# Performance work log

Hardware: AMD Instinct MI355X
Metric: run time of the kernel (lower is better)

Reference implementation:

```python
import jax, jax.numpy as jnp
import numpy as np

B, S, H, NH, HD = 2, 2048, 2048, 32, 64
ROPE_THETA = 10000.0


def _rope_tables(seq_len, head_dim, theta):
    inv_freq = 1.0 / (theta ** (jnp.arange(0, head_dim, 2, dtype=jnp.float32) / head_dim))
    t = jnp.arange(seq_len, dtype=jnp.float32)
    freqs = jnp.outer(t, inv_freq)                 # [S, HD/2]
    emb = jnp.concatenate([freqs, freqs], axis=-1)  # [S, HD]
    return jnp.cos(emb), jnp.sin(emb)


def setup_inputs() -> dict:
    key = jax.random.key(0)
    ks = jax.random.split(key, 6)
    cos, sin = _rope_tables(S, HD, ROPE_THETA)
    scale = 0.02
    return {
        "hidden_states": jax.random.normal(ks[0], (B, S, H), dtype=jnp.float32),
        "attention_mask": jnp.zeros((B, S), dtype=jnp.float32),
        "cos": cos,
        "sin": sin,
        "Wq": jax.random.normal(ks[1], (H, H), dtype=jnp.float32) * scale,
        "Wk": jax.random.normal(ks[2], (H, H), dtype=jnp.float32) * scale,
        "Wv": jax.random.normal(ks[3], (H, H), dtype=jnp.float32) * scale,
        "Wo": jax.random.normal(ks[4], (H, H), dtype=jnp.float32) * scale,
    }


def _rotate_half(x):
    x1, x2 = jnp.split(x, 2, axis=-1)
    return jnp.concatenate([-x2, x1], axis=-1)


def reference(hidden_states, attention_mask, cos, sin, Wq, Wk, Wv, Wo):
    b, s, _ = hidden_states.shape
    # QKV projections (nn.Linear: x @ W.T), reshape to [B, NH, S, HD]
    def proj(W):
        y = hidden_states @ W.T
        return y.reshape(b, s, NH, HD).transpose(0, 2, 1, 3)
    q, k, v = proj(Wq), proj(Wk), proj(Wv)
    # RoPE (HF rotate_half convention); cos/sin: [S, HD] -> broadcast [1,1,S,HD]
    c = cos[None, None, :, :]
    sn = sin[None, None, :, :]
    q = q * c + _rotate_half(q) * sn
    k = k * c + _rotate_half(k) * sn
    # attention: [B, NH, S, S]
    scores = jnp.einsum("bhqd,bhkd->bhqk", q, k) / jnp.sqrt(jnp.float32(HD))
    scores = scores + attention_mask[:, None, None, :]
    probs = jax.nn.softmax(scores, axis=-1)
    out = jnp.einsum("bhqk,bhkd->bhqd", probs, v)
    out = out.transpose(0, 2, 1, 3).reshape(b, s, NH * HD)
    return out @ Wo.T
```

## Files before the change

kernel.cpp:

```cpp
#include <hip/hip_runtime.h>
#include <stdint.h>
#include <math.h>

#define NB 2
#define SS 2048
#define HH 2048
#define NHH 32
#define HDD 64
#define MM (NB*SS)

typedef __attribute__((ext_vector_type(8))) short short8;
typedef __attribute__((ext_vector_type(4))) short short4v;
typedef __attribute__((ext_vector_type(4))) float f32x4;

#define GLOBAL_AS const __attribute__((address_space(1))) void*
#define LDS_AS __attribute__((address_space(3))) void*

static __device__ __forceinline__ short rne_bf16(float x) {
    uint32_t u = __builtin_bit_cast(uint32_t, x);
    u += 0x7FFFu + ((u >> 16) & 1u);
    return (short)(u >> 16);
}
static __device__ __forceinline__ float bf16f(short h) {
    return __builtin_bit_cast(float, (uint32_t)((uint16_t)h) << 16);
}
static __device__ __forceinline__ uint32_t cvt_pk_bf16(float a, float b) {
    uint32_t r;
    asm("v_cvt_pk_bf16_f32 %0, %1, %2" : "=v"(r) : "v"(a), "v"(b));
    return r;
}
static __device__ __forceinline__ float fast_exp2(float x) {
    float r;
    asm("v_exp_f32 %0, %1" : "=v"(r) : "v"(x));
    return r;
}

#define N4X  2097152
#define N4W  1048576
__global__ void __launch_bounds__(256)
k_cvt_all(const float* __restrict__ X, const float* __restrict__ Wq,
          const float* __restrict__ Wk, const float* __restrict__ Wv,
          const float* __restrict__ Wo,
          short* __restrict__ Xh, short* __restrict__ Wqh, short* __restrict__ Wkh,
          short* __restrict__ Wvh, short* __restrict__ Woh, short* __restrict__ Wol)
{
    int i = blockIdx.x * blockDim.x + threadIdx.x;
    const float* src;
    short* dst;
    int j = i;
    if (i < N4X)                { src = X;  dst = Xh;  }
    else if (i < N4X + N4W)     { src = Wq; dst = Wqh; j = i - N4X; }
    else if (i < N4X + 2*N4W)   { src = Wk; dst = Wkh; j = i - N4X - N4W; }
    else if (i < N4X + 3*N4W)   { src = Wv; dst = Wvh; j = i - N4X - 2*N4W; }
    else {
        j = i - N4X - 3*N4W;
        float4 f = reinterpret_cast<const float4*>(Wo)[j];
        short4v h, l;
        h.x = rne_bf16(f.x); l.x = rne_bf16(f.x - bf16f(h.x));
        h.y = rne_bf16(f.y); l.y = rne_bf16(f.y - bf16f(h.y));
        h.z = rne_bf16(f.z); l.z = rne_bf16(f.z - bf16f(h.z));
        h.w = rne_bf16(f.w); l.w = rne_bf16(f.w - bf16f(h.w));
        reinterpret_cast<short4v*>(Woh)[j] = h;
        reinterpret_cast<short4v*>(Wol)[j] = l;
        return;
    }
    float4 f = reinterpret_cast<const float4*>(src)[j];
    short4v o;
    o.x = rne_bf16(f.x); o.y = rne_bf16(f.y);
    o.z = rne_bf16(f.z); o.w = rne_bf16(f.w);
    reinterpret_cast<short4v*>(dst)[j] = o;
}

__global__ void __launch_bounds__(256, 2)
k_gemm_qkv(const short* __restrict__ X,
           const short* __restrict__ Wqh, const short* __restrict__ Wkh, const short* __restrict__ Wvh,
           const float* __restrict__ cosT, const float* __restrict__ sinT,
           short* __restrict__ Qr, short* __restrict__ Kr, short* __restrict__ Vt)
{
    __shared__ short lA[128 * 64];
    __shared__ short lBq[128 * 64];
    __shared__ short lBk[128 * 64];
    __shared__ short lBv[128 * 64];
    const int tid = threadIdx.x;
    const int lane = tid & 63;
    const int wave = tid >> 6;
    const int lrow = lane & 15;
    const int quad = lane >> 4;
    const int swz = lrow & 7;

    const int lin = blockIdx.y * 16 + blockIdx.x;
    const int pos = lin >> 3;
    const int nblk = ((lin & 7) * 2 + (pos & 1)) * 128;
    const int mblk = (pos >> 1) * 128;
    const int m0 = mblk + (wave >> 1) * 64;
    const int n0 = nblk + (wave & 1) * 64;
    const int mw = (wave >> 1) * 64;
    const int nw = (wave & 1) * 64;

    const int srow = wave * 32 + (lane >> 3);
    const int skc = ((lane & 7) ^ (lane >> 3)) * 8;
    const short* gA = X   + (size_t)(mblk + srow) * HH + skc;
    const short* gQ = Wqh + (size_t)(nblk + srow) * HH + skc;
    const short* gK = Wkh + (size_t)(nblk + srow) * HH + skc;
    const short* gV = Wvh + (size_t)(nblk + srow) * HH + skc;
    const int lofs = wave * 2048;

    f32x4 acc[3][4][4];
    #pragma unroll
    for (int z = 0; z < 3; z++)
        #pragma unroll
        for (int i = 0; i < 4; i++)
            #pragma unroll
            for (int j = 0; j < 4; j++) acc[z][i][j] = 0.f;

    #pragma unroll 1
    for (int k0 = 0; k0 < HH; k0 += 64) {
        __syncthreads();
        #pragma unroll
        for (int j = 0; j < 4; j++) {
            size_t go = (size_t)j * 8 * HH + k0;
            int lo = lofs + j * 512;
            __builtin_amdgcn_global_load_lds((GLOBAL_AS)(gA + go), (LDS_AS)(&lA[lo]),  16, 0, 0);
            __builtin_amdgcn_global_load_lds((GLOBAL_AS)(gQ + go), (LDS_AS)(&lBq[lo]), 16, 0, 0);
            __builtin_amdgcn_global_load_lds((GLOBAL_AS)(gK + go), (LDS_AS)(&lBk[lo]), 16, 0, 0);
            __builtin_amdgcn_global_load_lds((GLOBAL_AS)(gV + go), (LDS_AS)(&lBv[lo]), 16, 0, 0);
        }
        __syncthreads();

        const short* lBz[3] = { lBq, lBk, lBv };
        #pragma unroll
        for (int kk = 0; kk < 2; kk++) {
            const int csl = ((kk * 4 + quad) ^ swz) * 8;
            short8 a[4];
            #pragma unroll
            for (int mt = 0; mt < 4; mt++)
                a[mt] = *reinterpret_cast<const short8*>(&lA[(mw + mt * 16 + lrow) * 64 + csl]);
            #pragma unroll
            for (int z = 0; z < 3; z++) {
                short8 b[4];
                #pragma unroll
                for (int nt = 0; nt < 4; nt++)
                    b[nt] = *reinterpret_cast<const short8*>(&lBz[z][(nw + nt * 16 + lrow) * 64 + csl]);
                #pragma unroll
                for (int mt = 0; mt < 4; mt++)
                    #pragma unroll
                    for (int nt = 0; nt < 4; nt++)
                        acc[z][mt][nt] = __builtin_amdgcn_mfma_f32_16x16x32_bf16(a[mt], b[nt], acc[z][mt][nt], 0, 0, 0);
            }
        }
    }

    const float QSCL = 0.18033688011112042f;

    #pragma unroll
    for (int z = 0; z < 3; z++) {
        #pragma unroll
        for (int mt = 0; mt < 4; mt++) {
            #pragma unroll
            for (int r = 0; r < 4; r++) {
                int row = m0 + mt * 16 + quad * 4 + r;
                int b_i = row >> 11;
                int s_i = row & (SS - 1);
                #pragma unroll
                for (int nt = 0; nt < 4; nt++) {
                    int col = n0 + nt * 16 + lrow;
                    int h_i = col >> 6;
                    int d_i = col & 63;
                    float v = acc[z][mt][nt][r];
                    if (z < 2) {
                        float pair = (nt & 2) ? acc[z][mt][nt - 2][r] : -acc[z][mt][nt + 2][r];
                        float c = cosT[s_i * HDD + d_i];
                        float sn = sinT[s_i * HDD + d_i];
                        v = v * c + pair * sn;
                        if (z == 0) v *= QSCL;
                        short* dst = (z == 0) ? Qr : Kr;
                        dst[(((size_t)b_i * NHH + h_i) * SS + s_i) * HDD + d_i] = rne_bf16(v);
                    } else {
                        Vt[(((size_t)b_i * NHH + h_i) * HDD + d_i) * SS + s_i] = rne_bf16(v);
                    }
                }
            }
        }
    }
}

__global__ void __launch_bounds__(256, 2)
k_attn(const short* __restrict__ Qr, const short* __restrict__ Kr, const short* __restrict__ Vt,
       const float* __restrict__ mask,
       short* __restrict__ Ah, short* __restrict__ Al)
{
    __shared__ short plds[4][4096];
    __shared__ short ldsK[2][4096];
    __shared__ short ldsV[2][4096];
    const int lane = threadIdx.x & 63;
    const int wave = threadIdx.x >> 6;
    const int lrow = lane & 15;
    const int quad = lane >> 4;
    const int aofs = lrow & 7;
    const int b = blockIdx.x >> 5;
    const int h = blockIdx.x & 31;
    const int q0w = blockIdx.y * 256 + wave * 64;

    const size_t bh = (size_t)b * NHH + h;
    const short* Qbase = Qr + bh * SS * HDD;
    const short* Kbase = Kr + bh * SS * HDD;
    const short* Vbase = Vt + bh * (size_t)HDD * SS;
    const float* mrow = mask + b * SS;
    char* cb = (char*)&plds[wave][0];

    const int strow = lane >> 3;
    const int stch  = (lane & 7) ^ strow;
    const short* Kst0 = Kbase + (size_t)(wave * 16 + strow)     * HDD + stch * 8;
    const short* Kst1 = Kbase + (size_t)(wave * 16 + 8 + strow) * HDD + stch * 8;
    const short* Vst0 = Vbase + (size_t)(wave * 16 + strow)     * SS  + stch * 8;
    const short* Vst1 = Vbase + (size_t)(wave * 16 + 8 + strow) * SS  + stch * 8;
    const int ldst0 = wave * 1024;
    const int ldst1 = wave * 1024 + 512;

#define STAGE_KV(buf, kk) do { \
    __builtin_amdgcn_global_load_lds((GLOBAL_AS)(Kst0 + (size_t)(kk) * HDD), (LDS_AS)(&ldsK[buf][ldst0]), 16, 0, 0); \
    __builtin_amdgcn_global_load_lds((GLOBAL_AS)(Kst1 + (size_t)(kk) * HDD), (LDS_AS)(&ldsK[buf][ldst1]), 16, 0, 0); \
    __builtin_amdgcn_global_load_lds((GLOBAL_AS)(Vst0 + (kk)), (LDS_AS)(&ldsV[buf][ldst0]), 16, 0, 0); \
    __builtin_amdgcn_global_load_lds((GLOBAL_AS)(Vst1 + (kk)), (LDS_AS)(&ldsV[buf][ldst1]), 16, 0, 0); \
} while (0)

    short8 qf[4][2];
    #pragma unroll
    for (int nt = 0; nt < 4; nt++)
        #pragma unroll
        for (int c = 0; c < 2; c++)
            qf[nt][c] = *reinterpret_cast<const short8*>(
                Qbase + (size_t)(q0w + nt * 16 + lrow) * HDD + c * 32 + quad * 8);

    short8 onesf;
    #pragma unroll
    for (int i = 0; i < 8; i++) onesf[i] = (short)0x3F80;

    f32x4 oacc[4][4];
    f32x4 lacc[4];
    #pragma unroll
    for (int i = 0; i < 4; i++) {
        lacc[i] = 0.f;
        #pragma unroll
        for (int j = 0; j < 4; j++) oacc[i][j] = 0.f;
    }

    const float L2E = 1.44269504f;

    STAGE_KV(0, 0);
    asm volatile("s_waitcnt vmcnt(0)" ::: "memory");
    __syncthreads();

    int cur = 0;
    #pragma unroll 1
    for (int k0 = 0; k0 < SS; k0 += 64) {
        if (k0 + 64 < SS) STAGE_KV(cur ^ 1, k0 + 64);

        short8 kf[4][2];
        #pragma unroll
        for (int kt = 0; kt < 4; kt++)
            #pragma unroll
            for (int c = 0; c < 2; c++)
                kf[kt][c] = *reinterpret_cast<const short8*>(
                    &ldsK[cur][(kt * 16 + lrow) * 64 + (((4 * c + quad) ^ aofs) * 8)]);

        f32x4 sacc[4][4];
        #pragma unroll
        for (int kt = 0; kt < 4; kt++)
            #pragma unroll
            for (int nt = 0; nt < 4; nt++) {
                f32x4 z4 = 0.f;
                z4 = __builtin_amdgcn_mfma_f32_16x16x32_bf16(kf[kt][0], qf[nt][0], z4, 0, 0, 0);
                sacc[kt][nt] = __builtin_amdgcn_mfma_f32_16x16x32_bf16(kf[kt][1], qf[nt][1], z4, 0, 0, 0);
            }

        asm volatile("s_waitcnt lgkmcnt(0)" ::: "memory");

        #pragma unroll
        for (int kt = 0; kt < 4; kt++) {
            float4 mk = *reinterpret_cast<const float4*>(mrow + k0 + kt * 16 + quad * 4);
            float m0v = mk.x * L2E, m1v = mk.y * L2E, m2v = mk.z * L2E, m3v = mk.w * L2E;
            #pragma unroll
            for (int nt = 0; nt < 4; nt++) {
                float p0 = fast_exp2(sacc[kt][nt][0] + m0v);
                float p1 = fast_exp2(sacc[kt][nt][1] + m1v);
                float p2 = fast_exp2(sacc[kt][nt][2] + m2v);
                float p3 = fast_exp2(sacc[kt][nt][3] + m3v);
                uint2 w;
                w.x = cvt_pk_bf16(p0, p1);
                w.y = cvt_pk_bf16(p2, p3);
                *reinterpret_cast<uint2*>(
                    cb + (nt * 16 + lrow) * 128 +
                    (((2 * kt + (quad >> 1)) ^ aofs) * 16) + (quad & 1) * 8) = w;
            }
        }

        asm volatile("s_waitcnt lgkmcnt(0)" ::: "memory");

        #pragma unroll
        for (int c = 0; c < 2; c++) {
            short8 pf[4], vf[4];
            #pragma unroll
            for (int mt = 0; mt < 4; mt++)
                pf[mt] = *reinterpret_cast<const short8*>(
                    cb + (mt * 16 + lrow) * 128 + (((4 * c + quad) ^ aofs) * 16));
            #pragma unroll
            for (int dt = 0; dt < 4; dt++)
                vf[dt] = *reinterpret_cast<const short8*>(
                    &ldsV[cur][(dt * 16 + lrow) * 64 + (((4 * c + quad) ^ aofs) * 8)]);
            #pragma unroll
            for (int mt = 0; mt < 4; mt++) {
                lacc[mt] = __builtin_amdgcn_mfma_f32_16x16x32_bf16(pf[mt], onesf, lacc[mt], 0, 0, 0);
                #pragma unroll
                for (int dt = 0; dt < 4; dt++)
                    oacc[mt][dt] = __builtin_amdgcn_mfma_f32_16x16x32_bf16(pf[mt], vf[dt], oacc[mt][dt], 0, 0, 0);
            }
        }

        asm volatile("s_waitcnt vmcnt(0)" ::: "memory");
        __syncthreads();
        cur ^= 1;
    }
#undef STAGE_KV

    float linv[4][4];
    #pragma unroll
    for (int mt = 0; mt < 4; mt++)
        #pragma unroll
        for (int r = 0; r < 4; r++)
            linv[mt][r] = 1.f / lacc[mt][r];

    #pragma unroll
    for (int mt = 0; mt < 4; mt++) {
        #pragma unroll
        for (int r = 0; r < 4; r++) {
            int s_i = q0w + mt * 16 + quad * 4 + r;
            size_t row = (size_t)b * SS + s_i;
            #pragma unroll
            for (int dt = 0; dt < 4; dt++) {
                float x = oacc[mt][dt][r] * linv[mt][r];
                short hi = rne_bf16(x);
                short lo = rne_bf16(x - bf16f(hi));
                size_t idx = row * HH + (size_t)h * 64 + dt * 16 + lrow;
                Ah[idx] = hi;
                Al[idx] = lo;
            }
        }
    }
}

__global__ void __launch_bounds__(256, 2)
k_gemm_wo(const short* __restrict__ Ahh, const short* __restrict__ All,
          const short* __restrict__ Bhh, const short* __restrict__ Bll,
          float* __restrict__ C)
{
    __shared__ short lAh[128 * 64];
    __shared__ short lAl[128 * 64];
    __shared__ short lBh[128 * 64];
    __shared__ short lBl[128 * 64];
    const int tid = threadIdx.x;
    const int lane = tid & 63;
    const int wave = tid >> 6;
    const int lrow = lane & 15;
    const int quad = lane >> 4;
    const int swz = lrow & 7;

    const int lin = blockIdx.y * 16 + blockIdx.x;
    const int pos = lin >> 3;
    const int nblk = ((lin & 7) * 2 + (pos & 1)) * 128;
    const int mblk = (pos >> 1) * 128;
    const int m0 = mblk + (wave >> 1) * 64;
    const int n0 = nblk + (wave & 1) * 64;
    const int mw = (wave >> 1) * 64;
    const int nw = (wave & 1) * 64;

    const int srow = wave * 32 + (lane >> 3);
    const int skc = ((lane & 7) ^ (lane >> 3)) * 8;
    const short* gAh = Ahh + (size_t)(mblk + srow) * HH + skc;
    const short* gAl = All + (size_t)(mblk + srow) * HH + skc;
    const short* gBh = Bhh + (size_t)(nblk + srow) * HH + skc;
    const short* gBl = Bll + (size_t)(nblk + srow) * HH + skc;
    short* lAhw = &lAh[wave * 2048];
    short* lAlw = &lAl[wave * 2048];
    short* lBhw = &lBh[wave * 2048];
    short* lBlw = &lBl[wave * 2048];

    f32x4 acc[4][4];
    #pragma unroll
    for (int i = 0; i < 4; i++)
        #pragma unroll
        for (int j = 0; j < 4; j++) acc[i][j] = 0.f;

    #pragma unroll 1
    for (int k0 = 0; k0 < HH; k0 += 64) {
        __syncthreads();
        #pragma unroll
        for (int j = 0; j < 4; j++) {
            size_t go = (size_t)j * 8 * HH + k0;
            __builtin_amdgcn_global_load_lds((GLOBAL_AS)(gAh + go), (LDS_AS)(lAhw + j * 512), 16, 0, 0);
            __builtin_amdgcn_global_load_lds((GLOBAL_AS)(gAl + go), (LDS_AS)(lAlw + j * 512), 16, 0, 0);
            __builtin_amdgcn_global_load_lds((GLOBAL_AS)(gBh + go), (LDS_AS)(lBhw + j * 512), 16, 0, 0);
            __builtin_amdgcn_global_load_lds((GLOBAL_AS)(gBl + go), (LDS_AS)(lBlw + j * 512), 16, 0, 0);
        }
        __syncthreads();

        #pragma unroll
        for (int kk = 0; kk < 2; kk++) {
            const int csl = ((kk * 4 + quad) ^ swz) * 8;
            short8 ah[4], al[4], bh[4], bl[4];
            #pragma unroll
            for (int mt = 0; mt < 4; mt++) {
                int off = (mw + mt * 16 + lrow) * 64 + csl;
                ah[mt] = *reinterpret_cast<const short8*>(&lAh[off]);
                al[mt] = *reinterpret_cast<const short8*>(&lAl[off]);
            }
            #pragma unroll
            for (int nt = 0; nt < 4; nt++) {
                int off = (nw + nt * 16 + lrow) * 64 + csl;
                bh[nt] = *reinterpret_cast<const short8*>(&lBh[off]);
                bl[nt] = *reinterpret_cast<const short8*>(&lBl[off]);
            }
            #pragma unroll
            for (int mt = 0; mt < 4; mt++)
                #pragma unroll
                for (int nt = 0; nt < 4; nt++) {
                    acc[mt][nt] = __builtin_amdgcn_mfma_f32_16x16x32_bf16(ah[mt], bh[nt], acc[mt][nt], 0, 0, 0);
                    acc[mt][nt] = __builtin_amdgcn_mfma_f32_16x16x32_bf16(al[mt], bh[nt], acc[mt][nt], 0, 0, 0);
                    acc[mt][nt] = __builtin_amdgcn_mfma_f32_16x16x32_bf16(ah[mt], bl[nt], acc[mt][nt], 0, 0, 0);
                }
        }
    }

    #pragma unroll
    for (int mt = 0; mt < 4; mt++)
        #pragma unroll
        for (int r = 0; r < 4; r++) {
            int row = m0 + mt * 16 + quad * 4 + r;
            #pragma unroll
            for (int nt = 0; nt < 4; nt++) {
                int col = n0 + nt * 16 + lrow;
                C[(size_t)row * HH + col] = acc[mt][nt][r];
            }
        }
}

extern "C" void kernel_launch(void* const* d_in, const int* in_sizes, int n_in,
                              void* d_out, int out_size, void* d_ws, size_t ws_size,
                              hipStream_t stream) {
    const float* hidden = (const float*)d_in[0];
    const float* maskp  = (const float*)d_in[1];
    const float* cosT   = (const float*)d_in[2];
    const float* sinT   = (const float*)d_in[3];
    const float* Wq     = (const float*)d_in[4];
    const float* Wk     = (const float*)d_in[5];
    const float* Wv     = (const float*)d_in[6];
    const float* Wo     = (const float*)d_in[7];
    float* out = (float*)d_out;

    char* ws = (char*)d_ws;
    auto alloc = [&](size_t bytes) {
        char* p = ws;
        ws += (bytes + 255) & ~(size_t)255;
        return p;
    };
    const size_t XB = (size_t)MM * HH * sizeof(short);
    const size_t WB = (size_t)HH * HH * sizeof(short);
    short* Xh  = (short*)alloc(XB);
    short* Wqh = (short*)alloc(WB);
    short* Wkh = (short*)alloc(WB);
    short* Wvh = (short*)alloc(WB);
    short* Woh = (short*)alloc(WB);
    short* Wol = (short*)alloc(WB);
    short* Qr  = (short*)alloc(XB);
    short* Kr  = (short*)alloc(XB);
    short* Vt  = (short*)alloc(XB);
    short* Ah  = (short*)alloc(XB);
    short* Al  = (short*)alloc(XB);

    const int nAll = N4X + 4 * N4W;
    k_cvt_all<<<dim3(nAll / 256), dim3(256), 0, stream>>>(
        hidden, Wq, Wk, Wv, Wo, Xh, Wqh, Wkh, Wvh, Woh, Wol);

    k_gemm_qkv<<<dim3(HH / 128, MM / 128), dim3(256), 0, stream>>>(
        Xh, Wqh, Wkh, Wvh, cosT, sinT, Qr, Kr, Vt);

    k_attn<<<dim3(NB * NHH, SS / 256), dim3(256), 0, stream>>>(
        Qr, Kr, Vt, maskp, Ah, Al);

    k_gemm_wo<<<dim3(HH / 128, MM / 128), dim3(256), 0, stream>>>(
        Ah, Al, Woh, Wol, out);
}
```

Baseline: 402.3 us.

## Double-buffer LDS tiles in QKV and Wo GEMMs with k-step 32 prefetch

Both projection GEMMs now keep two LDS buffers of 32-wide K slices. The next slice is issued with global_load_lds before the MFMAs on the current slice run, so global latency overlaps compute instead of stalling between two barriers. The K step halves, which doubles the number of loop iterations and barriers, and the swizzle pattern is redone for the 32-column layout. Total LDS use stays the same.

```diff
diff --git a/kernel.cpp b/kernel.cpp
--- a/kernel.cpp
+++ b/kernel.cpp
@@ -77,16 +77,15 @@
            const float* __restrict__ cosT, const float* __restrict__ sinT,
            short* __restrict__ Qr, short* __restrict__ Kr, short* __restrict__ Vt)
 {
-    __shared__ short lA[128 * 64];
-    __shared__ short lBq[128 * 64];
-    __shared__ short lBk[128 * 64];
-    __shared__ short lBv[128 * 64];
+    __shared__ short lA[2][128 * 32];
+    __shared__ short lBq[2][128 * 32];
+    __shared__ short lBk[2][128 * 32];
+    __shared__ short lBv[2][128 * 32];
     const int tid = threadIdx.x;
     const int lane = tid & 63;
     const int wave = tid >> 6;
     const int lrow = lane & 15;
     const int quad = lane >> 4;
-    const int swz = lrow & 7;
 
     const int lin = blockIdx.y * 16 + blockIdx.x;
     const int pos = lin >> 3;
@@ -97,13 +96,25 @@
     const int mw = (wave >> 1) * 64;
     const int nw = (wave & 1) * 64;
 
-    const int srow = wave * 32 + (lane >> 3);
-    const int skc = ((lane & 7) ^ (lane >> 3)) * 8;
+    const int srow = wave * 16 + (lane >> 2);
+    const int skc = ((lane & 3) ^ ((lane >> 3) & 3)) * 8;
     const short* gA = X   + (size_t)(mblk + srow) * HH + skc;
     const short* gQ = Wqh + (size_t)(nblk + srow) * HH + skc;
     const short* gK = Wkh + (size_t)(nblk + srow) * HH + skc;
     const short* gV = Wvh + (size_t)(nblk + srow) * HH + skc;
-    const int lofs = wave * 2048;
+    const int lofs = wave * 512;
+
+#define STAGE_QKV(buf, kk) do { \
+    _Pragma("unroll") \
+    for (int j = 0; j < 2; j++) { \
+        size_t go = (size_t)j * 64 * HH + (kk); \
+        int lo = lofs + j * 2048; \
+        __builtin_amdgcn_global_load_lds((GLOBAL_AS)(gA + go), (LDS_AS)(&lA[buf][lo]),  16, 0, 0); \
+        __builtin_amdgcn_global_load_lds((GLOBAL_AS)(gQ + go), (LDS_AS)(&lBq[buf][lo]), 16, 0, 0); \
+        __builtin_amdgcn_global_load_lds((GLOBAL_AS)(gK + go), (LDS_AS)(&lBk[buf][lo]), 16, 0, 0); \
+        __builtin_amdgcn_global_load_lds((GLOBAL_AS)(gV + go), (LDS_AS)(&lBv[buf][lo]), 16, 0, 0); \
+    } \
+} while (0)
 
     f32x4 acc[3][4][4];
     #pragma unroll
@@ -113,42 +124,41 @@
             #pragma unroll
             for (int j = 0; j < 4; j++) acc[z][i][j] = 0.f;
 
+    const int slot = (quad ^ ((lrow >> 1) & 3)) * 8;
+
+    STAGE_QKV(0, 0);
+    asm volatile("s_waitcnt vmcnt(0)" ::: "memory");
+    __syncthreads();
+
+    int cur = 0;
     #pragma unroll 1
-    for (int k0 = 0; k0 < HH; k0 += 64) {
-        __syncthreads();
-        #pragma unroll
-        for (int j = 0; j < 4; j++) {
-            size_t go = (size_t)j * 8 * HH + k0;
-            int lo = lofs + j * 512;
-            __builtin_amdgcn_global_load_lds((GLOBAL_AS)(gA + go), (LDS_AS)(&lA[lo]),  16, 0, 0);
-            __builtin_amdgcn_global_load_lds((GLOBAL_AS)(gQ + go), (LDS_AS)(&lBq[lo]), 16, 0, 0);
-            __builtin_amdgcn_global_load_lds((GLOBAL_AS)(gK + go), (LDS_AS)(&lBk[lo]), 16, 0, 0);
-            __builtin_amdgcn_global_load_lds((GLOBAL_AS)(gV + go), (LDS_AS)(&lBv[lo]), 16, 0, 0);
-        }
-        __syncthreads();
-
-        const short* lBz[3] = { lBq, lBk, lBv };
-        #pragma unroll
-        for (int kk = 0; kk < 2; kk++) {
-            const int csl = ((kk * 4 + quad) ^ swz) * 8;
-            short8 a[4];
+    for (int k0 = 0; k0 < HH; k0 += 32) {
+        if (k0 + 32 < HH) STAGE_QKV(cur ^ 1, k0 + 32);
+
+        short8 a[4];
+        #pragma unroll
+        for (int mt = 0; mt < 4; mt++)
+            a[mt] = *reinterpret_cast<const short8*>(&lA[cur][(mw + mt * 16 + lrow) * 32 + slot]);
+
+        const short* lBz[3] = { &lBq[cur][0], &lBk[cur][0], &lBv[cur][0] };
+        #pragma unroll
+        for (int z = 0; z < 3; z++) {
+            short8 b[4];
+            #pragma unroll
+            for (int nt = 0; nt < 4; nt++)
+                b[nt] = *reinterpret_cast<const short8*>(&lBz[z][(nw + nt * 16 + lrow) * 32 + slot]);
             #pragma unroll
             for (int mt = 0; mt < 4; mt++)
-                a[mt] = *reinterpret_cast<const short8*>(&lA[(mw + mt * 16 + lrow) * 64 + csl]);
-            #pragma unroll
-            for (int z = 0; z < 3; z++) {
-                short8 b[4];
                 #pragma unroll
                 for (int nt = 0; nt < 4; nt++)
-                    b[nt] = *reinterpret_cast<const short8*>(&lBz[z][(nw + nt * 16 + lrow) * 64 + csl]);
-                #pragma unroll
-                for (int mt = 0; mt < 4; mt++)
-                    #pragma unroll
-                    for (int nt = 0; nt < 4; nt++)
-                        acc[z][mt][nt] = __builtin_amdgcn_mfma_f32_16x16x32_bf16(a[mt], b[nt], acc[z][mt][nt], 0, 0, 0);
-            }
-        }
-    }
+                    acc[z][mt][nt] = __builtin_amdgcn_mfma_f32_16x16x32_bf16(a[mt], b[nt], acc[z][mt][nt], 0, 0, 0);
+        }
+
+        asm volatile("s_waitcnt vmcnt(0)" ::: "memory");
+        __syncthreads();
+        cur ^= 1;
+    }
+#undef STAGE_QKV
 
     const float QSCL = 0.18033688011112042f;
 
@@ -354,16 +364,15 @@
           const short* __restrict__ Bhh, const short* __restrict__ Bll,
           float* __restrict__ C)
 {
-    __shared__ short lAh[128 * 64];
-    __shared__ short lAl[128 * 64];
-    __shared__ short lBh[128 * 64];
-    __shared__ short lBl[128 * 64];
+    __shared__ short lAh[2][128 * 32];
+    __shared__ short lAl[2][128 * 32];
+    __shared__ short lBh[2][128 * 32];
+    __shared__ short lBl[2][128 * 32];
     const int tid = threadIdx.x;
     const int lane = tid & 63;
     const int wave = tid >> 6;
     const int lrow = lane & 15;
     const int quad = lane >> 4;
-    const int swz = lrow & 7;
 
     const int lin = blockIdx.y * 16 + blockIdx.x;
     const int pos = lin >> 3;
@@ -374,16 +383,25 @@
     const int mw = (wave >> 1) * 64;
     const int nw = (wave & 1) * 64;
 
-    const int srow = wave * 32 + (lane >> 3);
-    const int skc = ((lane & 7) ^ (lane >> 3)) * 8;
+    const int srow = wave * 16 + (lane >> 2);
+    const int skc = ((lane & 3) ^ ((lane >> 3) & 3)) * 8;
     const short* gAh = Ahh + (size_t)(mblk + srow) * HH + skc;
     const short* gAl = All + (size_t)(mblk + srow) * HH + skc;
     const short* gBh = Bhh + (size_t)(nblk + srow) * HH + skc;
     const short* gBl = Bll + (size_t)(nblk + srow) * HH + skc;
-    short* lAhw = &lAh[wave * 2048];
-    short* lAlw = &lAl[wave * 2048];
-    short* lBhw = &lBh[wave * 2048];
-    short* lBlw = &lBl[wave * 2048];
+    const int lofs = wave * 512;
+
+#define STAGE_WO(buf, kk) do { \
+    _Pragma("unroll") \
+    for (int j = 0; j < 2; j++) { \
+        size_t go = (size_t)j * 64 * HH + (kk); \
+        int lo = lofs + j * 2048; \
+        __builtin_amdgcn_global_load_lds((GLOBAL_AS)(gAh + go), (LDS_AS)(&lAh[buf][lo]), 16, 0, 0); \
+        __builtin_amdgcn_global_load_lds((GLOBAL_AS)(gAl + go), (LDS_AS)(&lAl[buf][lo]), 16, 0, 0); \
+        __builtin_amdgcn_global_load_lds((GLOBAL_AS)(gBh + go), (LDS_AS)(&lBh[buf][lo]), 16, 0, 0); \
+        __builtin_amdgcn_global_load_lds((GLOBAL_AS)(gBl + go), (LDS_AS)(&lBl[buf][lo]), 16, 0, 0); \
+    } \
+} while (0)
 
     f32x4 acc[4][4];
     #pragma unroll
@@ -391,45 +409,44 @@
         #pragma unroll
         for (int j = 0; j < 4; j++) acc[i][j] = 0.f;
 
+    const int slot = (quad ^ ((lrow >> 1) & 3)) * 8;
+
+    STAGE_WO(0, 0);
+    asm volatile("s_waitcnt vmcnt(0)" ::: "memory");
+    __syncthreads();
+
+    int cur = 0;
     #pragma unroll 1
-    for (int k0 = 0; k0 < HH; k0 += 64) {
+    for (int k0 = 0; k0 < HH; k0 += 32) {
+        if (k0 + 32 < HH) STAGE_WO(cur ^ 1, k0 + 32);
+
+        short8 ah[4], al[4], bh[4], bl[4];
+        #pragma unroll
+        for (int mt = 0; mt < 4; mt++) {
+            int off = (mw + mt * 16 + lrow) * 32 + slot;
+            ah[mt] = *reinterpret_cast<const short8*>(&lAh[cur][off]);
+            al[mt] = *reinterpret_cast<const short8*>(&lAl[cur][off]);
+        }
+        #pragma unroll
+        for (int nt = 0; nt < 4; nt++) {
+            int off = (nw + nt * 16 + lrow) * 32 + slot;
+            bh[nt] = *reinterpret_cast<const short8*>(&lBh[cur][off]);
+            bl[nt] = *reinterpret_cast<const short8*>(&lBl[cur][off]);
+        }
+        #pragma unroll
+        for (int mt = 0; mt < 4; mt++)
+            #pragma unroll
+            for (int nt = 0; nt < 4; nt++) {
+                acc[mt][nt] = __builtin_amdgcn_mfma_f32_16x16x32_bf16(ah[mt], bh[nt], acc[mt][nt], 0, 0, 0);
+                acc[mt][nt] = __builtin_amdgcn_mfma_f32_16x16x32_bf16(al[mt], bh[nt], acc[mt][nt], 0, 0, 0);
+                acc[mt][nt] = __builtin_amdgcn_mfma_f32_16x16x32_bf16(ah[mt], bl[nt], acc[mt][nt], 0, 0, 0);
+            }
+
+        asm volatile("s_waitcnt vmcnt(0)" ::: "memory");
         __syncthreads();
-        #pragma unroll
-        for (int j = 0; j < 4; j++) {
-            size_t go = (size_t)j * 8 * HH + k0;
-            __builtin_amdgcn_global_load_lds((GLOBAL_AS)(gAh + go), (LDS_AS)(lAhw + j * 512), 16, 0, 0);
-            __builtin_amdgcn_global_load_lds((GLOBAL_AS)(gAl + go), (LDS_AS)(lAlw + j * 512), 16, 0, 0);
-            __builtin_amdgcn_global_load_lds((GLOBAL_AS)(gBh + go), (LDS_AS)(lBhw + j * 512), 16, 0, 0);
-            __builtin_amdgcn_global_load_lds((GLOBAL_AS)(gBl + go), (LDS_AS)(lBlw + j * 512), 16, 0, 0);
-        }
-        __syncthreads();
-
-        #pragma unroll
-        for (int kk = 0; kk < 2; kk++) {
-            const int csl = ((kk * 4 + quad) ^ swz) * 8;
-            short8 ah[4], al[4], bh[4], bl[4];
-            #pragma unroll
-            for (int mt = 0; mt < 4; mt++) {
-                int off = (mw + mt * 16 + lrow) * 64 + csl;
-                ah[mt] = *reinterpret_cast<const short8*>(&lAh[off]);
-                al[mt] = *reinterpret_cast<const short8*>(&lAl[off]);
-            }
-            #pragma unroll
-            for (int nt = 0; nt < 4; nt++) {
-                int off = (nw + nt * 16 + lrow) * 64 + csl;
-                bh[nt] = *reinterpret_cast<const short8*>(&lBh[off]);
-                bl[nt] = *reinterpret_cast<const short8*>(&lBl[off]);
-            }
-            #pragma unroll
-            for (int mt = 0; mt < 4; mt++)
-                #pragma unroll
-                for (int nt = 0; nt < 4; nt++) {
-                    acc[mt][nt] = __builtin_amdgcn_mfma_f32_16x16x32_bf16(ah[mt], bh[nt], acc[mt][nt], 0, 0, 0);
-                    acc[mt][nt] = __builtin_amdgcn_mfma_f32_16x16x32_bf16(al[mt], bh[nt], acc[mt][nt], 0, 0, 0);
-                    acc[mt][nt] = __builtin_amdgcn_mfma_f32_16x16x32_bf16(ah[mt], bl[nt], acc[mt][nt], 0, 0, 0);
-                }
-        }
-    }
+        cur ^= 1;
+    }
+#undef STAGE_WO
 
     #pragma unroll
     for (int mt = 0; mt < 4; mt++)
```

Measured after the change: 425.1 us. +5.7%, slower.

## Load GEMM weight operands directly from global memory instead of staging in LDS

Applied to the files above, without the earlier changes.

In the QKV and Wo projection GEMMs, the B (weight) tiles are no longer staged through shared memory. Each lane reads its MFMA B fragment straight from global memory with 16-byte vector loads, and only the activation tile stays in LDS. This cuts LDS footprint and LDS traffic, which may help occupancy, but it loses reuse across the two waves that share the same N columns. The global loads are also issued right before the MFMAs with no prefetching, so their latency is exposed.

```diff
diff --git a/kernel.cpp b/kernel.cpp
--- a/kernel.cpp
+++ b/kernel.cpp
@@ -78,9 +78,6 @@
            short* __restrict__ Qr, short* __restrict__ Kr, short* __restrict__ Vt)
 {
     __shared__ short lA[128 * 64];
-    __shared__ short lBq[128 * 64];
-    __shared__ short lBk[128 * 64];
-    __shared__ short lBv[128 * 64];
     const int tid = threadIdx.x;
     const int lane = tid & 63;
     const int wave = tid >> 6;
@@ -99,11 +96,16 @@
 
     const int srow = wave * 32 + (lane >> 3);
     const int skc = ((lane & 7) ^ (lane >> 3)) * 8;
-    const short* gA = X   + (size_t)(mblk + srow) * HH + skc;
-    const short* gQ = Wqh + (size_t)(nblk + srow) * HH + skc;
-    const short* gK = Wkh + (size_t)(nblk + srow) * HH + skc;
-    const short* gV = Wvh + (size_t)(nblk + srow) * HH + skc;
+    const short* gA = X + (size_t)(mblk + srow) * HH + skc;
     const int lofs = wave * 2048;
+
+    const short* Wz3[3] = { Wqh, Wkh, Wvh };
+    const short* bp[3][4];
+    #pragma unroll
+    for (int z = 0; z < 3; z++)
+        #pragma unroll
+        for (int nt = 0; nt < 4; nt++)
+            bp[z][nt] = Wz3[z] + (size_t)(nblk + nw + nt * 16 + lrow) * HH + quad * 8;
 
     f32x4 acc[3][4][4];
     #pragma unroll
@@ -117,17 +119,11 @@
     for (int k0 = 0; k0 < HH; k0 += 64) {
         __syncthreads();
         #pragma unroll
-        for (int j = 0; j < 4; j++) {
-            size_t go = (size_t)j * 8 * HH + k0;
-            int lo = lofs + j * 512;
-            __builtin_amdgcn_global_load_lds((GLOBAL_AS)(gA + go), (LDS_AS)(&lA[lo]),  16, 0, 0);
-            __builtin_amdgcn_global_load_lds((GLOBAL_AS)(gQ + go), (LDS_AS)(&lBq[lo]), 16, 0, 0);
-            __builtin_amdgcn_global_load_lds((GLOBAL_AS)(gK + go), (LDS_AS)(&lBk[lo]), 16, 0, 0);
-            __builtin_amdgcn_global_load_lds((GLOBAL_AS)(gV + go), (LDS_AS)(&lBv[lo]), 16, 0, 0);
-        }
+        for (int j = 0; j < 4; j++)
+            __builtin_amdgcn_global_load_lds((GLOBAL_AS)(gA + (size_t)j * 8 * HH + k0),
+                                             (LDS_AS)(&lA[lofs + j * 512]), 16, 0, 0);
         __syncthreads();
 
-        const short* lBz[3] = { lBq, lBk, lBv };
         #pragma unroll
         for (int kk = 0; kk < 2; kk++) {
             const int csl = ((kk * 4 + quad) ^ swz) * 8;
@@ -140,7 +136,7 @@
                 short8 b[4];
                 #pragma unroll
                 for (int nt = 0; nt < 4; nt++)
-                    b[nt] = *reinterpret_cast<const short8*>(&lBz[z][(nw + nt * 16 + lrow) * 64 + csl]);
+                    b[nt] = *reinterpret_cast<const short8*>(bp[z][nt] + k0 + kk * 32);
                 #pragma unroll
                 for (int mt = 0; mt < 4; mt++)
                     #pragma unroll
@@ -356,8 +352,6 @@
 {
     __shared__ short lAh[128 * 64];
     __shared__ short lAl[128 * 64];
-    __shared__ short lBh[128 * 64];
-    __shared__ short lBl[128 * 64];
     const int tid = threadIdx.x;
     const int lane = tid & 63;
     const int wave = tid >> 6;
@@ -378,12 +372,16 @@
     const int skc = ((lane & 7) ^ (lane >> 3)) * 8;
     const short* gAh = Ahh + (size_t)(mblk + srow) * HH + skc;
     const short* gAl = All + (size_t)(mblk + srow) * HH + skc;
-    const short* gBh = Bhh + (size_t)(nblk + srow) * HH + skc;
-    const short* gBl = Bll + (size_t)(nblk + srow) * HH + skc;
-    short* lAhw = &lAh[wave * 2048];
-    short* lAlw = &lAl[wave * 2048];
-    short* lBhw = &lBh[wave * 2048];
-    short* lBlw = &lBl[wave * 2048];
+    const int lofs = wave * 2048;
+
+    const short* bph[4];
+    const short* bpl[4];
+    #pragma unroll
+    for (int nt = 0; nt < 4; nt++) {
+        size_t rofs = (size_t)(nblk + nw + nt * 16 + lrow) * HH + quad * 8;
+        bph[nt] = Bhh + rofs;
+        bpl[nt] = Bll + rofs;
+    }
 
     f32x4 acc[4][4];
     #pragma unroll
@@ -397,10 +395,8 @@
         #pragma unroll
         for (int j = 0; j < 4; j++) {
             size_t go = (size_t)j * 8 * HH + k0;
-            __builtin_amdgcn_global_load_lds((GLOBAL_AS)(gAh + go), (LDS_AS)(lAhw + j * 512), 16, 0, 0);
-            __builtin_amdgcn_global_load_lds((GLOBAL_AS)(gAl + go), (LDS_AS)(lAlw + j * 512), 16, 0, 0);
-            __builtin_amdgcn_global_load_lds((GLOBAL_AS)(gBh + go), (LDS_AS)(lBhw + j * 512), 16, 0, 0);
-            __builtin_amdgcn_global_load_lds((GLOBAL_AS)(gBl + go), (LDS_AS)(lBlw + j * 512), 16, 0, 0);
+            __builtin_amdgcn_global_load_lds((GLOBAL_AS)(gAh + go), (LDS_AS)(&lAh[lofs + j * 512]), 16, 0, 0);
+            __builtin_amdgcn_global_load_lds((GLOBAL_AS)(gAl + go), (LDS_AS)(&lAl[lofs + j * 512]), 16, 0, 0);
         }
         __syncthreads();
 
@@ -416,9 +412,8 @@
             }
             #pragma unroll
             for (int nt = 0; nt < 4; nt++) {
-                int off = (nw + nt * 16 + lrow) * 64 + csl;
-                bh[nt] = *reinterpret_cast<const short8*>(&lBh[off]);
-                bl[nt] = *reinterpret_cast<const short8*>(&lBl[off]);
+                bh[nt] = *reinterpret_cast<const short8*>(bph[nt] + k0 + kk * 32);
+                bl[nt] = *reinterpret_cast<const short8*>(bpl[nt] + k0 + kk * 32);
             }
             #pragma unroll
             for (int mt = 0; mt < 4; mt++)
```

After: 575.4 us. +43.0%, slower.
